# Kernel optimization log

Measured on AMD Instinct MI355X. Metric: run time of the kernel, lower is better.

Reference implementation:

```python
import jax, jax.numpy as jnp
import numpy as np

C = 64
CR = C // 16  # reduction=16 -> query/key channels
B, H, W = 2, 80, 80


def setup_inputs() -> dict:
    key = jax.random.key(0)
    ks = jax.random.split(key, 13)
    s = 0.05
    return {
        "a": jax.random.normal(ks[0], (B, C, H, W), jnp.float32),
        "b": jax.random.normal(ks[1], (B, C, H, W), jnp.float32),
        "c": jax.random.normal(ks[2], (B, C, H, W), jnp.float32),
        # attentionAB (queries from a, keys from b)
        "wq_ab": jax.random.normal(ks[3], (CR, C), jnp.float32) * s,
        "bq_ab": jax.random.normal(ks[4], (CR,), jnp.float32) * s,
        "wk_ab": jax.random.normal(ks[5], (CR, C), jnp.float32) * s,
        "bk_ab": jax.random.normal(ks[6], (CR,), jnp.float32) * s,
        # attentionBC (queries from c, keys from b)
        "wq_bc": jax.random.normal(ks[7], (CR, C), jnp.float32) * s,
        "bq_bc": jax.random.normal(ks[8], (CR,), jnp.float32) * s,
        "wk_bc": jax.random.normal(ks[9], (CR, C), jnp.float32) * s,
        "bk_bc": jax.random.normal(ks[10], (CR,), jnp.float32) * s,
        # outer value conv on b
        "wv": jax.random.normal(ks[11], (C, C), jnp.float32) * s,
        "bv": jax.random.normal(ks[12], (C,), jnp.float32) * s,
    }


def _proj(x_flat, w, bias):
    # conv1x1 on flattened [B, C, N] -> [B, D, N]
    return jnp.einsum("dc,bcn->bdn", w, x_flat) + bias[None, :, None]


def _attention(x1_flat, x2_flat, wq, bq, wk, bk):
    q = _proj(x1_flat, wq, bq)  # [B, CR, N1]
    k = _proj(x2_flat, wk, bk)  # [B, CR, N2]
    scores = jnp.einsum("bdn,bdm->bnm", q, k)  # [B, N1, N2]
    return jax.nn.softmax(scores, axis=-1)


def reference(a, b, c, wq_ab, bq_ab, wk_ab, bk_ab, wq_bc, bq_bc, wk_bc, bk_bc, wv, bv):
    bsz, ch, h, w = b.shape
    n = h * w
    af = a.reshape(bsz, ch, n)
    bf = b.reshape(bsz, ch, n)
    cf = c.reshape(bsz, ch, n)

    attn_ba = _attention(af, bf, wq_ab, bq_ab, wk_ab, bk_ab)  # [B, Na, Nb]
    attn_bc = _attention(cf, bf, wq_bc, bq_bc, wk_bc, bk_bc)  # [B, Nc, Nb]

    values_b = _proj(bf, wv, bv)  # [B, C, Nb]

    # bmm(values_b, attn^T): contract over key positions m (of b)
    enh_ba = jnp.einsum("bcm,bnm->bcn", values_b, attn_ba)
    enh_bc = jnp.einsum("bcm,bnm->bcn", values_b, attn_bc)
    enhanced = (enh_ba + enh_bc) * 0.5
    return enhanced.reshape(bsz, ch, h, w)
```

## Files before the change

kernel.cpp:

```cpp
#include <hip/hip_runtime.h>
#include <hip/hip_bf16.h>

#define NPIX 6400
#define LOG2E 1.44269504088896340736f
#define KH 5
#define KEYS 1280
#define NCH 20
#define QF 2
#define VSTRIDE 136

typedef _Float16 half_t;
typedef _Float16 half4 __attribute__((ext_vector_type(4)));
typedef float float4x __attribute__((ext_vector_type(4)));
typedef unsigned long long u64;

__global__ __launch_bounds__(256) void proj_kernel(
    const float* __restrict__ a, const float* __restrict__ b, const float* __restrict__ c,
    const float* __restrict__ wq_ab, const float* __restrict__ bq_ab,
    const float* __restrict__ wk_ab, const float* __restrict__ bk_ab,
    const float* __restrict__ wq_bc, const float* __restrict__ bq_bc,
    const float* __restrict__ wk_bc, const float* __restrict__ bk_bc,
    const float* __restrict__ wv, const float* __restrict__ bvb,
    half_t* __restrict__ qp, half_t* __restrict__ kp, half_t* __restrict__ vp)
{
    int bid = blockIdx.x;
    if (bid < 400) {
        int tid = bid * 256 + threadIdx.x;
        int n4 = tid % 1600;
        int cc = (tid / 1600) & 31;
        int bz = tid / (1600 * 32);
        const float* B = b + bz * 64 * NPIX + n4 * 4;
        float b0 = bvb[cc], b1 = bvb[cc + 32];
        float4x acc0 = {b0, b0, b0, b0}, acc1 = {b1, b1, b1, b1};
        for (int ch = 0; ch < 64; ++ch) {
            float4x bv = *(const float4x*)(B + ch * NPIX);
            acc0 += wv[cc * 64 + ch] * bv;
            acc1 += wv[(cc + 32) * 64 + ch] * bv;
        }
        half4 h0 = {(half_t)acc0[0], (half_t)acc0[1], (half_t)acc0[2], (half_t)acc0[3]};
        half4 h1 = {(half_t)acc1[0], (half_t)acc1[1], (half_t)acc1[2], (half_t)acc1[3]};
        *(half4*)(vp + (bz * 64 + cc) * NPIX + n4 * 4) = h0;
        *(half4*)(vp + (bz * 64 + cc + 32) * NPIX + n4 * 4) = h1;
    } else {
        int tid = (bid - 400) * 256 + threadIdx.x;
        int d = tid & 3;
        int n = (tid >> 2) % NPIX;
        int bz = (tid >> 2) / NPIX;
        const float* A = a + bz * 64 * NPIX + n;
        const float* B = b + bz * 64 * NPIX + n;
        const float* C = c + bz * 64 * NPIX + n;
        float qab = 0.f, kab = 0.f, qbc = 0.f, kbc = 0.f;
#pragma unroll 4
        for (int ch = 0; ch < 64; ++ch) {
            float av = A[ch * NPIX], bv = B[ch * NPIX], cv = C[ch * NPIX];
            qab += wq_ab[d * 64 + ch] * av;
            kab += wk_ab[d * 64 + ch] * bv;
            qbc += wq_bc[d * 64 + ch] * cv;
            kbc += wk_bc[d * 64 + ch] * bv;
        }
        qp[((bz * 2 + 0) * NPIX + n) * 4 + d] = (half_t)((qab + bq_ab[d]) * LOG2E);
        qp[((bz * 2 + 1) * NPIX + n) * 4 + d] = (half_t)((qbc + bq_bc[d]) * LOG2E);
        kp[((bz * 2 + 0) * NPIX + n) * 4 + d] = (half_t)(kab + bk_ab[d]);
        kp[((bz * 2 + 1) * NPIX + n) * 4 + d] = (half_t)(kbc + bk_bc[d]);
    }
}

__global__ __launch_bounds__(256) void attn_kernel(
    const half_t* __restrict__ qp, const half_t* __restrict__ kp,
    const half_t* __restrict__ vp, float* __restrict__ num, float* __restrict__ lsum)
{
    int bid = blockIdx.x;
    int swz = (bid & 7) * 125 + (bid >> 3);
    int qc = swz % 50;
    int br = (swz / 50) & 1;
    int bz = (swz / 100) & 1;
    int kh = swz / 200;

    int tid = threadIdx.x;
    int lane = tid & 63, w = tid >> 6;
    int g = lane >> 4, qi = lane & 15;
    int qbase = qc * 128 + w * 32;

    const half_t* Q = qp + ((bz * 2 + br) * NPIX + qbase) * 4;
    const half_t* K = kp + ((bz * 2 + br) * NPIX + kh * KEYS) * 4;
    const half_t* V = vp + bz * 64 * NPIX + kh * KEYS;

    half4 hz = {(half_t)0, (half_t)0, (half_t)0, (half_t)0};
    half4 qf[QF];
#pragma unroll
    for (int i = 0; i < QF; ++i)
        qf[i] = (lane < 16) ? *(const half4*)(Q + (i * 16 + lane) * 4) : hz;

    float4x accs[QF][4] = {{{0,0,0,0},{0,0,0,0},{0,0,0,0},{0,0,0,0}},
                           {{0,0,0,0},{0,0,0,0},{0,0,0,0},{0,0,0,0}}};
    float lrun[QF] = {0.f, 0.f};

    __shared__ char lds[2][64 * VSTRIDE];

    u64 vpre[4];
#pragma unroll
    for (int p = 0; p < 4; ++p) {
        int idx = p * 256 + tid; int row = idx >> 4, w4 = idx & 15;
        vpre[p] = *(const u64*)(V + row * NPIX + w4 * 4);
    }
    half4 kc[4];
#pragma unroll
    for (int t = 0; t < 4; ++t)
        kc[t] = (lane < 16) ? *(const half4*)(K + (t * 16 + lane) * 4) : hz;
#pragma unroll
    for (int p = 0; p < 4; ++p) {
        int idx = p * 256 + tid; int row = idx >> 4, w4 = idx & 15;
        *(u64*)(lds[0] + row * VSTRIDE + w4 * 8) = vpre[p];
    }
    __syncthreads();

    int cur = 0;
    for (int chn = 0; chn < NCH; ++chn) {
        bool more = (chn + 1 < NCH);
        u64 vn[4];
        half4 kn[4];
        if (more) {
            int m0n = (chn + 1) * 64;
#pragma unroll
            for (int p = 0; p < 4; ++p) {
                int idx = p * 256 + tid; int row = idx >> 4, w4 = idx & 15;
                vn[p] = *(const u64*)(V + row * NPIX + m0n + w4 * 4);
            }
#pragma unroll
            for (int t = 0; t < 4; ++t)
                kn[t] = (lane < 16) ? *(const half4*)(K + (m0n + t * 16 + lane) * 4) : hz;
        }
        const char* lb = lds[cur];
#pragma unroll
        for (int t = 0; t < 4; ++t) {
            half4 vf[4];
#pragma unroll
            for (int cb = 0; cb < 4; ++cb)
                vf[cb] = *(const half4*)(lb + (cb * 16 + qi) * VSTRIDE + t * 32 + g * 8);
#pragma unroll
            for (int i = 0; i < QF; ++i) {
                float4x zero = {0.f, 0.f, 0.f, 0.f};
                float4x sc = __builtin_amdgcn_mfma_f32_16x16x16f16(kc[t], qf[i], zero, 0, 0, 0);
                float p0 = exp2f(sc[0]), p1 = exp2f(sc[1]), p2 = exp2f(sc[2]), p3 = exp2f(sc[3]);
                lrun[i] += (p0 + p1) + (p2 + p3);
                half4 pf = {(half_t)p0, (half_t)p1, (half_t)p2, (half_t)p3};
#pragma unroll
                for (int cb = 0; cb < 4; ++cb)
                    accs[i][cb] = __builtin_amdgcn_mfma_f32_16x16x16f16(vf[cb], pf, accs[i][cb], 0, 0, 0);
            }
        }
        if (more) {
#pragma unroll
            for (int p = 0; p < 4; ++p) {
                int idx = p * 256 + tid; int row = idx >> 4, w4 = idx & 15;
                *(u64*)(lds[cur ^ 1] + row * VSTRIDE + w4 * 8) = vn[p];
            }
#pragma unroll
            for (int t = 0; t < 4; ++t) kc[t] = kn[t];
        }
        __syncthreads();
        cur ^= 1;
    }

    float* numb = num + (bz * 2 + br) * 64 * NPIX;
#pragma unroll
    for (int i = 0; i < QF; ++i) {
        float l = lrun[i];
        l += __shfl_xor(l, 16, 64);
        l += __shfl_xor(l, 32, 64);
        int q = qbase + i * 16 + qi;
        if (g == 0) atomicAdd(&lsum[(bz * 2 + br) * NPIX + q], l);
#pragma unroll
        for (int cb = 0; cb < 4; ++cb)
#pragma unroll
            for (int r = 0; r < 4; ++r)
                atomicAdd(&numb[(cb * 16 + 4 * g + r) * NPIX + q], accs[i][cb][r]);
    }
}

__global__ __launch_bounds__(256) void norm_kernel(
    const float* __restrict__ num, const float* __restrict__ lsum, float* __restrict__ out)
{
    int tid = blockIdx.x * 256 + threadIdx.x;
    int n4 = tid % 1600;
    int c  = (tid / 1600) & 63;
    int bz = tid / (1600 * 64);
    float4x lA = *(const float4x*)(lsum + (bz * 2 + 0) * NPIX + n4 * 4);
    float4x lC = *(const float4x*)(lsum + (bz * 2 + 1) * NPIX + n4 * 4);
    float4x vA = *(const float4x*)(num + ((bz * 2 + 0) * 64 + c) * NPIX + n4 * 4);
    float4x vC = *(const float4x*)(num + ((bz * 2 + 1) * 64 + c) * NPIX + n4 * 4);
    float4x r;
#pragma unroll
    for (int j = 0; j < 4; ++j)
        r[j] = 0.5f * (vA[j] * __builtin_amdgcn_rcpf(lA[j]) +
                       vC[j] * __builtin_amdgcn_rcpf(lC[j]));
    *(float4x*)(out + (bz * 64 + c) * NPIX + n4 * 4) = r;
}

extern "C" void kernel_launch(void* const* d_in, const int* in_sizes, int n_in,
                              void* d_out, int out_size, void* d_ws, size_t ws_size,
                              hipStream_t stream) {
    (void)in_sizes; (void)n_in; (void)out_size; (void)ws_size;
    const float* a     = (const float*)d_in[0];
    const float* b     = (const float*)d_in[1];
    const float* c     = (const float*)d_in[2];
    const float* wq_ab = (const float*)d_in[3];
    const float* bq_ab = (const float*)d_in[4];
    const float* wk_ab = (const float*)d_in[5];
    const float* bk_ab = (const float*)d_in[6];
    const float* wq_bc = (const float*)d_in[7];
    const float* bq_bc = (const float*)d_in[8];
    const float* wk_bc = (const float*)d_in[9];
    const float* bk_bc = (const float*)d_in[10];
    const float* wv    = (const float*)d_in[11];
    const float* bv    = (const float*)d_in[12];
    float* out = (float*)d_out;

    half_t* qp = (half_t*)d_ws;
    half_t* kp = qp + 2 * 2 * NPIX * 4;
    half_t* vp = kp + 2 * 2 * NPIX * 4;
    float* num  = (float*)(vp + 2 * 64 * NPIX);
    float* lsum = num + 2 * 2 * 64 * NPIX;

    hipMemsetAsync(num, 0, (size_t)(2 * 2 * 64 * NPIX + 2 * 2 * NPIX) * sizeof(float), stream);

    proj_kernel<<<600, 256, 0, stream>>>(a, b, c, wq_ab, bq_ab, wk_ab, bk_ab,
                                         wq_bc, bq_bc, wk_bc, bk_bc, wv, bv, qp, kp, vp);
    attn_kernel<<<1000, 256, 0, stream>>>(qp, kp, vp, num, lsum);
    norm_kernel<<<800, 256, 0, stream>>>(num, lsum, out);
}
```

Baseline: 199.5 us.

## Fold zeroing into proj kernel, fast exp2, packed cvt, double-buffer LDS V reads

```diff
diff --git a/kernel.cpp b/kernel.cpp
--- a/kernel.cpp
+++ b/kernel.cpp
@@ -11,8 +11,15 @@
 
 typedef _Float16 half_t;
 typedef _Float16 half4 __attribute__((ext_vector_type(4)));
+typedef __fp16 fp16x2 __attribute__((ext_vector_type(2)));
 typedef float float4x __attribute__((ext_vector_type(4)));
 typedef unsigned long long u64;
+
+__device__ __forceinline__ float fast_exp2(float x) {
+    float r;
+    asm volatile("v_exp_f32 %0, %1" : "=v"(r) : "v"(x));
+    return r;
+}
 
 __global__ __launch_bounds__(256) void proj_kernel(
     const float* __restrict__ a, const float* __restrict__ b, const float* __restrict__ c,
@@ -21,7 +28,8 @@
     const float* __restrict__ wq_bc, const float* __restrict__ bq_bc,
     const float* __restrict__ wk_bc, const float* __restrict__ bk_bc,
     const float* __restrict__ wv, const float* __restrict__ bvb,
-    half_t* __restrict__ qp, half_t* __restrict__ kp, half_t* __restrict__ vp)
+    half_t* __restrict__ qp, half_t* __restrict__ kp, half_t* __restrict__ vp,
+    float* __restrict__ num)
 {
     int bid = blockIdx.x;
     if (bid < 400) {
@@ -41,7 +49,7 @@
         half4 h1 = {(half_t)acc1[0], (half_t)acc1[1], (half_t)acc1[2], (half_t)acc1[3]};
         *(half4*)(vp + (bz * 64 + cc) * NPIX + n4 * 4) = h0;
         *(half4*)(vp + (bz * 64 + cc + 32) * NPIX + n4 * 4) = h1;
-    } else {
+    } else if (bid < 600) {
         int tid = (bid - 400) * 256 + threadIdx.x;
         int d = tid & 3;
         int n = (tid >> 2) % NPIX;
@@ -62,6 +70,11 @@
         qp[((bz * 2 + 1) * NPIX + n) * 4 + d] = (half_t)((qbc + bq_bc[d]) * LOG2E);
         kp[((bz * 2 + 0) * NPIX + n) * 4 + d] = (half_t)(kab + bk_ab[d]);
         kp[((bz * 2 + 1) * NPIX + n) * 4 + d] = (half_t)(kbc + bk_bc[d]);
+    } else {
+        int tid = (bid - 600) * 256 + threadIdx.x;
+        float4x z = {0.f, 0.f, 0.f, 0.f};
+        float4x* p = (float4x*)num;
+        for (int i = tid; i < 416000; i += 25600) p[i] = z;
     }
 }
 
@@ -131,22 +144,33 @@
                 kn[t] = (lane < 16) ? *(const half4*)(K + (m0n + t * 16 + lane) * 4) : hz;
         }
         const char* lb = lds[cur];
+        half4 vfa[4], vfb[4];
+#pragma unroll
+        for (int cb = 0; cb < 4; ++cb)
+            vfa[cb] = *(const half4*)(lb + (cb * 16 + qi) * VSTRIDE + g * 8);
 #pragma unroll
         for (int t = 0; t < 4; ++t) {
-            half4 vf[4];
-#pragma unroll
-            for (int cb = 0; cb < 4; ++cb)
-                vf[cb] = *(const half4*)(lb + (cb * 16 + qi) * VSTRIDE + t * 32 + g * 8);
+            half4* vcur = (t & 1) ? vfb : vfa;
+            half4* vnxt = (t & 1) ? vfa : vfb;
+            if (t < 3) {
+#pragma unroll
+                for (int cb = 0; cb < 4; ++cb)
+                    vnxt[cb] = *(const half4*)(lb + (cb * 16 + qi) * VSTRIDE + (t + 1) * 32 + g * 8);
+            }
 #pragma unroll
             for (int i = 0; i < QF; ++i) {
                 float4x zero = {0.f, 0.f, 0.f, 0.f};
                 float4x sc = __builtin_amdgcn_mfma_f32_16x16x16f16(kc[t], qf[i], zero, 0, 0, 0);
-                float p0 = exp2f(sc[0]), p1 = exp2f(sc[1]), p2 = exp2f(sc[2]), p3 = exp2f(sc[3]);
+                float p0 = fast_exp2(sc[0]), p1 = fast_exp2(sc[1]);
+                float p2 = fast_exp2(sc[2]), p3 = fast_exp2(sc[3]);
                 lrun[i] += (p0 + p1) + (p2 + p3);
-                half4 pf = {(half_t)p0, (half_t)p1, (half_t)p2, (half_t)p3};
+                union { fp16x2 h2[2]; half4 h4; } pk;
+                pk.h2[0] = __builtin_amdgcn_cvt_pkrtz(p0, p1);
+                pk.h2[1] = __builtin_amdgcn_cvt_pkrtz(p2, p3);
+                half4 pf = pk.h4;
 #pragma unroll
                 for (int cb = 0; cb < 4; ++cb)
-                    accs[i][cb] = __builtin_amdgcn_mfma_f32_16x16x16f16(vf[cb], pf, accs[i][cb], 0, 0, 0);
+                    accs[i][cb] = __builtin_amdgcn_mfma_f32_16x16x16f16(vcur[cb], pf, accs[i][cb], 0, 0, 0);
             }
         }
         if (more) {
@@ -222,10 +246,9 @@
     float* num  = (float*)(vp + 2 * 64 * NPIX);
     float* lsum = num + 2 * 2 * 64 * NPIX;
 
-    hipMemsetAsync(num, 0, (size_t)(2 * 2 * 64 * NPIX + 2 * 2 * NPIX) * sizeof(float), stream);
-
-    proj_kernel<<<600, 256, 0, stream>>>(a, b, c, wq_ab, bq_ab, wk_ab, bk_ab,
-                                         wq_bc, bq_bc, wk_bc, bk_bc, wv, bv, qp, kp, vp);
+    proj_kernel<<<700, 256, 0, stream>>>(a, b, c, wq_ab, bq_ab, wk_ab, bk_ab,
+                                         wq_bc, bq_bc, wk_bc, bk_bc, wv, bv,
+                                         qp, kp, vp, num);
     attn_kernel<<<1000, 256, 0, stream>>>(qp, kp, vp, num, lsum);
     norm_kernel<<<800, 256, 0, stream>>>(num, lsum, out);
 }
```

Result: faster. 193.7 us (-2.9%).
